# Kernel optimization log

Hardware: AMD Instinct MI355X
Metric: run time of the kernel (lower is better)

## Reference

```python
import jax, jax.numpy as jnp
import numpy as np

DIM = 2048
H = 16           # n_heads
KV = 4           # n_kv_heads
G = H // KV      # gqa factor
CQ = 128         # q_compressed_dim
QN, QR = 96, 32  # q nope / rope head dims
CKV = 128        # kv_compressed_dim
KN, KR = 64, 64  # k nope / rope head dims
VD = 256         # v_head_dim
THETA = 10000.0


def _t5_layer_norm(x, gamma, eps=1e-5):
    mu = jnp.mean(x, axis=-1, keepdims=True)
    var = jnp.var(x, axis=-1, keepdims=True)
    return (x - mu) * jax.lax.rsqrt(var + eps) * gamma


def _rope(x):
    # x: [B, H, S, D] with interleaved even/odd rotation, positions = arange(S)
    S, D = x.shape[-2], x.shape[-1]
    inv_freq = 1.0 / THETA ** (jnp.arange(0, D, 2, dtype=jnp.float32) / D)
    ang = jnp.arange(S, dtype=jnp.float32)[:, None] * inv_freq  # [S, D/2]
    cos = jnp.cos(ang).astype(x.dtype)
    sin = jnp.sin(ang).astype(x.dtype)
    xe, xo = x[..., ::2], x[..., 1::2]
    re = xe * cos - xo * sin
    ro = xe * sin + xo * cos
    return jnp.stack((re, ro), axis=-1).reshape(x.shape)


def setup_inputs() -> dict:
    key = jax.random.key(0)
    ks = jax.random.split(key, 7)
    s = 0.02
    return {
        "x": jax.random.normal(ks[0], (2, 2048, DIM), dtype=jnp.float32),
        "w_dq": jax.random.normal(ks[1], (DIM, CQ), dtype=jnp.float32) * s,
        "gamma_q": jnp.ones((CQ,), dtype=jnp.float32),
        "w_uq": jax.random.normal(ks[2], (CQ, H * (QN + QR)), dtype=jnp.float32) * s,
        "w_dkv": jax.random.normal(ks[3], (DIM, CKV + KR), dtype=jnp.float32) * s,
        "gamma_kv": jnp.ones((CKV,), dtype=jnp.float32),
        "w_ukv": jax.random.normal(ks[4], (CKV, KV * (KN + VD)), dtype=jnp.float32) * s,
        "w_o": jax.random.normal(ks[5], (H * VD, DIM), dtype=jnp.float32) * s,
    }


def reference(x, w_dq, gamma_q, w_uq, w_dkv, gamma_kv, w_ukv, w_o):
    B, S, _ = x.shape
    # low-rank Q path
    cq = _t5_layer_norm(x @ w_dq, gamma_q)                     # [B,S,CQ]
    q = cq @ w_uq                                              # [B,S,H*(QN+QR)]
    q_nope = q[..., : H * QN].reshape(B, S, H, QN).transpose(0, 2, 1, 3)
    q_rope = q[..., H * QN :].reshape(B, S, H, QR).transpose(0, 2, 1, 3)
    q_rope = _rope(q_rope)
    q_states = jnp.concatenate((q_nope, q_rope), axis=-1)      # [B,H,S,QN+QR]

    # low-rank KV path + decoupled shared rope key
    ckv_kr = x @ w_dkv                                         # [B,S,CKV+KR]
    ckv = _t5_layer_norm(ckv_kr[..., :CKV], gamma_kv)
    k_rope = _rope(ckv_kr[..., CKV:][:, None, :, :])           # [B,1,S,KR]
    kv = ckv @ w_ukv                                           # [B,S,KV*(KN+VD)]
    k_nope = kv[..., : KV * KN].reshape(B, S, KV, KN).transpose(0, 2, 1, 3)
    v_states = kv[..., KV * KN :].reshape(B, S, KV, VD).transpose(0, 2, 1, 3)
    k_states = jnp.concatenate(
        (k_nope, jnp.broadcast_to(k_rope, (B, KV, S, KR))), axis=-1
    )                                                          # [B,KV,S,KN+KR]

    # grouped-query attention: broadcast kv heads instead of materializing repeats
    dqk = QN + QR  # == KN + KR == 128
    qg = q_states.reshape(B, KV, G, S, dqk)
    scores = jnp.einsum("bgrqd,bgkd->bgrqk", qg, k_states) / jnp.sqrt(
        jnp.asarray(dqk, dtype=x.dtype)
    )
    causal = jnp.triu(jnp.ones((S, S), dtype=bool), k=1)
    scores = jnp.where(causal, -jnp.inf, scores)
    attn = jax.nn.softmax(scores, axis=-1)
    out = jnp.einsum("bgrqk,bgkv->bgrqv", attn, v_states)      # [B,KV,G,S,VD]
    out = out.reshape(B, H, S, VD).transpose(0, 2, 1, 3).reshape(B, S, H * VD)
    return out @ w_o
```

## Files before the change

### kernel.cpp

```cpp
#include <hip/hip_runtime.h>
#include <hip/hip_bf16.h>
#include <math.h>

#define DIM   2048
#define S_LEN 2048
#define BATCH 2
#define NH    16
#define NKV   4
#define CQ_   128
#define QN_   96
#define QR_   32
#define CKV_  128
#define KN_   64
#define KR_   64
#define VD_   256
#define ROWS_TOT (BATCH*S_LEN)
#define QK_SCALE 0.08838834764831845f
#define LOG2E    1.4426950408889634f

typedef __attribute__((ext_vector_type(8)))  short short8;
typedef __attribute__((ext_vector_type(4)))  short short4v;
typedef __attribute__((ext_vector_type(4)))  float float4v;
typedef __attribute__((ext_vector_type(16))) float float16v;
typedef __attribute__((ext_vector_type(4)))  int   int4v;

__device__ inline short f2bf(float x) {
    union { __hip_bfloat16 h; short s; } u;
    u.h = __float2bfloat16(x);
    return u.s;
}

__device__ __forceinline__ void gl_lds16(const short* g, short* lds) {
    __builtin_amdgcn_global_load_lds(
        (const __attribute__((address_space(1))) unsigned int*)(g),
        (__attribute__((address_space(3))) unsigned int*)(lds),
        16, 0, 0);
}


__global__ __launch_bounds__(256)
void kprep_all(const float* __restrict__ x, const float* __restrict__ w_o,
               const float* __restrict__ w_uq, const float* __restrict__ w_ukv,
               const float* __restrict__ w_dq, const float* __restrict__ w_dkv,
               short* __restrict__ xbf, short* __restrict__ w_oT,
               short* __restrict__ w_uqT, short* __restrict__ w_ukvT,
               short* __restrict__ wdT, float* __restrict__ tq,
               float* __restrict__ tk)
{
    const int bid = blockIdx.x, tid = threadIdx.x;
    if (bid < 4096) {
        int i = bid * 2048 + tid * 8;
        float4 a = *reinterpret_cast<const float4*>(x + i);
        float4 b = *reinterpret_cast<const float4*>(x + i + 4);
        short8 o;
        o[0] = f2bf(a.x); o[1] = f2bf(a.y); o[2] = f2bf(a.z); o[3] = f2bf(a.w);
        o[4] = f2bf(b.x); o[5] = f2bf(b.y); o[6] = f2bf(b.z); o[7] = f2bf(b.w);
        *reinterpret_cast<short8*>(xbf + i) = o;
        return;
    }
    if (bid >= 6408) {
        int gid = (bid - 6408) * 256 + tid;
        int spos = gid / 48, e = gid - spos * 48;
        if (e < 16) {
            float inv = powf(10000.f, -(float)(2 * e) / 32.f);
            float sn, c; sincosf((float)spos * inv, &sn, &c);
            tq[(spos * 16 + e) * 2 + 0] = c;
            tq[(spos * 16 + e) * 2 + 1] = sn;
        } else {
            int i2 = e - 16;
            float inv = powf(10000.f, -(float)(2 * i2) / 64.f);
            float sn, c; sincosf((float)spos * inv, &sn, &c);
            tk[(spos * 32 + i2) * 2 + 0] = c;
            tk[(spos * 32 + i2) * 2 + 1] = sn;
        }
        return;
    }

    __shared__ float tf[64][65];
    const int tb = bid - 4096;
    int lb, nct, R; short* dst;
    if (tb < 2048)      { lb = tb;        nct = 32; R = 4096; dst = w_oT;   }
    else if (tb < 2112) { lb = tb - 2048; nct = 32; R = 128;  dst = w_uqT;  }
    else if (tb < 2152) { lb = tb - 2112; nct = 20; R = 128;  dst = w_ukvT; }
    else                { lb = tb - 2152; nct = 5;  R = 2048; dst = wdT;    }
    const int ct = lb % nct, rt = lb / nct;
    const int r0 = rt * 64, c0 = ct * 64;
    const float* src; int stride, nbase;
    if (tb < 2048)      { src = w_o;   stride = 2048; nbase = c0; }
    else if (tb < 2112) { src = w_uq;  stride = 2048; nbase = c0; }
    else if (tb < 2152) { src = w_ukv; stride = 1280; nbase = c0; }
    else if (ct < 2)    { src = w_dq;  stride = 128;  nbase = c0; }
    else                { src = w_dkv; stride = 192;  nbase = c0 - 128; }

    #pragma unroll
    for (int u4 = 0; u4 < 4; ++u4) {
        int u = u4 * 256 + tid;
        int kr = u >> 4, nc = (u & 15) * 4;
        float4 v = *reinterpret_cast<const float4*>(&src[(size_t)(r0 + kr) * stride + nbase + nc]);
        tf[kr][nc + 0] = v.x; tf[kr][nc + 1] = v.y;
        tf[kr][nc + 2] = v.z; tf[kr][nc + 3] = v.w;
    }
    __syncthreads();
    #pragma unroll
    for (int u2 = 0; u2 < 2; ++u2) {
        int u = u2 * 256 + tid;
        int nr = u >> 3, kc8 = (u & 7) * 8;
        short8 o;
        #pragma unroll
        for (int j = 0; j < 8; ++j) o[j] = f2bf(tf[kc8 + j][nr]);
        *reinterpret_cast<short8*>(&dst[(size_t)(c0 + nr) * R + r0 + kc8]) = o;
    }
}

__global__ __launch_bounds__(256)
void k1_mfma(const short* __restrict__ xbf, const short* __restrict__ wdT,
             const float* __restrict__ gamma_q, const float* __restrict__ gamma_kv,
             const float* __restrict__ tk,
             short* __restrict__ cq_bf, short* __restrict__ ckv_bf,
             float* __restrict__ kr_rope)
{
    __shared__ float ys[16][321];
    __shared__ float st[16][4];
    const int tid = threadIdx.x, lane = tid & 63, w = tid >> 6;
    const int g = lane >> 4, l15 = lane & 15;
    const int m0 = blockIdx.x * 16;
    const int wn0 = w * 80;

    float4v acc[5];
    #pragma unroll
    for (int nj = 0; nj < 5; ++nj) acc[nj] = (float4v){0.f, 0.f, 0.f, 0.f};

    const short* arow = xbf + (size_t)(m0 + l15) * 2048 + g * 8;
    for (int ks = 0; ks < 64; ++ks) {
        short8 a = *reinterpret_cast<const short8*>(arow + ks * 32);
        #pragma unroll
        for (int nj = 0; nj < 5; ++nj) {
            short8 bf = *reinterpret_cast<const short8*>(
                wdT + (size_t)(wn0 + nj * 16 + l15) * 2048 + ks * 32 + g * 8);
            acc[nj] = __builtin_amdgcn_mfma_f32_16x16x32_bf16(a, bf, acc[nj], 0, 0, 0);
        }
    }

    #pragma unroll
    for (int nj = 0; nj < 5; ++nj)
        #pragma unroll
        for (int r = 0; r < 4; ++r)
            ys[g * 4 + r][wn0 + nj * 16 + l15] = acc[nj][r];
    __syncthreads();

    if (tid < 32) {
        int row = tid >> 1, seg = tid & 1, base = seg * 128;
        float s1 = 0.f, s2 = 0.f;
        for (int j = 0; j < 128; ++j) { float v = ys[row][base + j]; s1 += v; s2 += v * v; }
        float mu  = s1 * (1.f / 128.f);
        float var = s2 * (1.f / 128.f) - mu * mu;
        st[row][seg * 2 + 0] = mu;
        st[row][seg * 2 + 1] = rsqrtf(var + 1e-5f);
    }
    __syncthreads();

    for (int i = tid; i < 16 * 320; i += 256) {
        int row = i / 320, col = i - row * 320;
        int r = m0 + row, spos = r & (S_LEN - 1);
        float v = ys[row][col];
        if (col < 128) {
            cq_bf[(size_t)r * CQ_ + col] =
                f2bf((v - st[row][0]) * st[row][1] * gamma_q[col] * (QK_SCALE * LOG2E));
        } else if (col < 256) {
            ckv_bf[(size_t)r * CKV_ + (col - 128)] =
                f2bf((v - st[row][2]) * st[row][3] * gamma_kv[col - 128]);
        } else {
            int d = col - 256, i2 = d >> 1;
            float xe = ys[row][256 + (d & ~1)];
            float xo = ys[row][256 + (d | 1)];
            float c  = tk[(spos * 32 + i2) * 2 + 0];
            float sn = tk[(spos * 32 + i2) * 2 + 1];
            kr_rope[(size_t)r * KR_ + d] = (d & 1) ? (xe * sn + xo * c)
                                                   : (xe * c - xo * sn);
        }
    }
}

__global__ __launch_bounds__(256)
void k23_fused(const short* __restrict__ cq_bf, const short* __restrict__ w_uqT,
               const float* __restrict__ tq, short* __restrict__ q_states,
               const short* __restrict__ ckv_bf, const short* __restrict__ w_ukvT,
               const float* __restrict__ kr_rope,
               short* __restrict__ k_frag, short* __restrict__ v_frag)
{
    const int tid = threadIdx.x, lane = tid & 63, w = tid >> 6;
    const int g = lane >> 4, l15 = lane & 15;

    if (blockIdx.x < 512) {
        const int bm = blockIdx.x >> 1, ns = blockIdx.x & 1;
        const int m0 = bm * 16;
        const int nb = ns * 1024 + w * 256;

        short8 af[4];
        #pragma unroll
        for (int ks = 0; ks < 4; ++ks)
            af[ks] = *reinterpret_cast<const short8*>(
                cq_bf + (size_t)(m0 + l15) * 128 + ks * 32 + g * 8);

        float4v acc[16];
        #pragma unroll
        for (int nj = 0; nj < 16; ++nj) acc[nj] = (float4v){0.f, 0.f, 0.f, 0.f};

        #pragma unroll
        for (int ks = 0; ks < 4; ++ks)
            #pragma unroll
            for (int nj = 0; nj < 16; ++nj) {
                short8 bf = *reinterpret_cast<const short8*>(
                    w_uqT + (size_t)(nb + nj * 16 + l15) * 128 + ks * 32 + g * 8);
                acc[nj] = __builtin_amdgcn_mfma_f32_16x16x32_bf16(af[ks], bf, acc[nj], 0, 0, 0);
            }

        #pragma unroll
        for (int nj = 0; nj < 16; ++nj) {
            int j = nb + nj * 16 + l15;
            if (j < NH * QN_) {
                int h = j / QN_, d = j - h * QN_;
                #pragma unroll
                for (int r = 0; r < 4; ++r) {
                    int rg = m0 + g * 4 + r, bb = rg >> 11, spos = rg & (S_LEN - 1);
                    q_states[(((size_t)bb * NH + h) * S_LEN + spos) * 128 + d] =
                        f2bf(acc[nj][r]);
                }
            } else {
                int jj = j - NH * QN_;
                int h = jj >> 5, d = jj & 31, i2 = d >> 1;
                #pragma unroll
                for (int r = 0; r < 4; ++r) {
                    int rg = m0 + g * 4 + r, bb = rg >> 11, spos = rg & (S_LEN - 1);
                    float v = acc[nj][r];
                    float p = __shfl_xor(v, 1, 64);
                    float c  = tq[(spos * 16 + i2) * 2 + 0];
                    float sn = tq[(spos * 16 + i2) * 2 + 1];
                    float out = (d & 1) ? (p * sn + v * c) : (v * c - p * sn);
                    q_states[(((size_t)bb * NH + h) * S_LEN + spos) * 128 + QN_ + d] =
                        f2bf(out);
                }
            }
        }
    } else {
        const int m0 = (blockIdx.x - 512) * 16;
        const int nb = w * 320;

        short8 af[4];
        #pragma unroll
        for (int ks = 0; ks < 4; ++ks)
            af[ks] = *reinterpret_cast<const short8*>(
                ckv_bf + (size_t)(m0 + l15) * 128 + ks * 32 + g * 8);

        float4v acc[20];
        #pragma unroll
        for (int nj = 0; nj < 20; ++nj) acc[nj] = (float4v){0.f, 0.f, 0.f, 0.f};

        #pragma unroll
        for (int ks = 0; ks < 4; ++ks)
            #pragma unroll
            for (int nj = 0; nj < 20; ++nj) {
                short8 bf = *reinterpret_cast<const short8*>(
                    w_ukvT + (size_t)(nb + nj * 16 + l15) * 128 + ks * 32 + g * 8);
                acc[nj] = __builtin_amdgcn_mfma_f32_16x16x32_bf16(af[ks], bf, acc[nj], 0, 0, 0);
            }

        #pragma unroll
        for (int nj = 0; nj < 20; ++nj) {
            int j = nb + nj * 16 + l15;
            if (j < NKV * KN_) {
                int kvh = j >> 6, d = j & 63;
                int stf = d >> 4, hif = (d >> 3) & 1, jo = d & 7;
                #pragma unroll
                for (int r = 0; r < 4; ++r) {
                    int rg = m0 + g * 4 + r, bb = rg >> 11, spos = rg & (S_LEN - 1);
                    int bk = bb * NKV + kvh;
                    size_t idx = ((size_t)(bk * 32 + (spos >> 6)) * 1024
                                  + ((spos >> 5) & 1) * 512 + stf * 64 + hif * 32
                                  + (spos & 31)) * 8 + jo;
                    k_frag[idx] = f2bf(acc[nj][r]);
                }
            } else {
                int jj = j - NKV * KN_;
                int kvh = jj >> 8, d = jj & 255;
                int dt5 = d >> 5, l31d = d & 31;
                #pragma unroll
                for (int r = 0; r < 4; ++r) {
                    int rg = m0 + g * 4 + r, bb = rg >> 11, spos = rg & (S_LEN - 1);
                    int bk = bb * NKV + kvh;
                    size_t slot = (size_t)(bk * 32 + (spos >> 6)) * 2048
                                  + dt5 * 256 + ((spos & 63) >> 5) * 128
                                  + ((spos >> 4) & 1) * 64 + ((spos >> 3) & 1) * 32 + l31d;
                    v_frag[slot * 8 + (spos & 7)] = f2bf(acc[nj][r]);
                }
            }
        }

        for (int i = tid; i < 16 * KR_; i += 256) {
            int rr = i >> 6, dd = i & 63;
            int rg = m0 + rr, bb = rg >> 11, spos = rg & (S_LEN - 1);
            short vv = f2bf(kr_rope[(size_t)rg * KR_ + dd]);
            int d = 64 + dd;
            int stf = d >> 4, hif = (d >> 3) & 1, jo = d & 7;
            size_t ubase = ((size_t)(spos >> 6)) * 1024
                           + ((spos >> 5) & 1) * 512 + stf * 64 + hif * 32 + (spos & 31);
            #pragma unroll
            for (int kvh = 0; kvh < NKV; ++kvh) {
                int bk = bb * NKV + kvh;
                k_frag[((size_t)bk * 32 * 1024 + ubase) * 8 + jo] = vv;
            }
        }
    }
}

__global__ __launch_bounds__(512, 1)
void k4_attn_mfma(const short* __restrict__ q_states,
                  const short* __restrict__ k_frag,
                  const short* __restrict__ v_frag,
                  short* __restrict__ attn_out)
{
    __shared__ __align__(16) short ks_lds[3][8192];
    __shared__ __align__(16) short vt_lds[2][16384];

    const int tid = threadIdx.x, lane = tid & 63, w = tid >> 6;
    const int l31 = lane & 31, hi = lane >> 5;
    const int g = w & 3, h = w >> 2;
    const int bid = blockIdx.x;
    const int qt = (bid < 256) ? (15 - (bid >> 5)) : (7 - ((bid - 256) >> 5));
    const int bh = bid & 31;
    const int h_head = bh & 15, b = bh >> 4, kvh = h_head >> 2;
    const int bk = b * NKV + kvh;

    const short* kfbase = k_frag + (size_t)bk * 32 * 8192;
    const short* vfbase = v_frag + (size_t)bk * 32 * 16384;

    const int qrow0 = qt * 128 + g * 32;
    const int qglob = qrow0 + l31;

    short8 qcur[8];
    {
        const short* qr = q_states +
            (((size_t)b * NH + h_head) * S_LEN + qrow0 + l31) * 128 + hi * 8;
        #pragma unroll
        for (int st = 0; st < 8; ++st)
            qcur[st] = *reinterpret_cast<const short8*>(qr + st * 16);
    }

    float16v o[8];
    #pragma unroll
    for (int dt = 0; dt < 8; ++dt)
        #pragma unroll
        for (int r = 0; r < 16; ++r) o[dt][r] = 0.f;
    float mreg = -1e30f, lreg = 0.f;

    const int nkt = 2 * (qt + 1);

    auto issueK = [&](int kt, int bufi) {
        const short* src = kfbase + (size_t)kt * 8192;
        #pragma unroll
        for (int i = 0; i < 2; ++i) {
            int c = w * 2 + i;
            gl_lds16(src + c * 512 + lane * 8, &ks_lds[bufi][c * 512]);
        }
    };
    auto issueV = [&](int kt, int bufi) {
        const short* src = vfbase + (size_t)kt * 16384;
        #pragma unroll
        for (int i = 0; i < 4; ++i) {
            int c = w * 4 + i;
            gl_lds16(src + c * 512 + lane * 8, &vt_lds[bufi][c * 512]);
        }
    };

    issueK(0, 0);
    issueV(0, 0);
    issueK(1, 1);

    for (int seq = 0; seq < nkt; ++seq) {
        if (seq < nkt - 1) { asm volatile("s_waitcnt vmcnt(2)" ::: "memory"); }
        else               { asm volatile("s_waitcnt vmcnt(0)" ::: "memory"); }
        __builtin_amdgcn_s_barrier();
        __builtin_amdgcn_sched_barrier(0);

        if (seq + 1 < nkt) issueV(seq + 1, (seq + 1) & 1);
        if (seq + 2 < nkt) issueK(seq + 2, (seq + 2) % 3);

        const int kvb = seq * 64 + h * 32;
        if (kvb <= qrow0 + 31) {
            const short* kbuf = &ks_lds[seq % 3][h * 4096];
            float16v sa, sb;
            #pragma unroll
            for (int r = 0; r < 16; ++r) { sa[r] = 0.f; sb[r] = 0.f; }
            __builtin_amdgcn_s_setprio(1);
            #pragma unroll
            for (int st = 0; st < 8; st += 2) {
                short8 kf0 = *reinterpret_cast<const short8*>(kbuf + st * 512 + lane * 8);
                sa = __builtin_amdgcn_mfma_f32_32x32x16_bf16(kf0, qcur[st], sa, 0, 0, 0);
                short8 kf1 = *reinterpret_cast<const short8*>(kbuf + (st + 1) * 512 + lane * 8);
                sb = __builtin_amdgcn_mfma_f32_32x32x16_bf16(kf1, qcur[st + 1], sb, 0, 0, 0);
            }
            __builtin_amdgcn_s_setprio(0);
            float16v s;
            #pragma unroll
            for (int r = 0; r < 16; ++r) s[r] = sa[r] + sb[r];

            if (kvb + 31 > qglob || kvb + 31 > qrow0 + 31) {
                if (kvb + 31 > qrow0) {
                    #pragma unroll
                    for (int r = 0; r < 16; ++r) {
                        int kc = kvb + ((r & 3) + 8 * (r >> 2) + 4 * hi);
                        if (kc > qglob) s[r] = -1e30f;
                    }
                }
            }

            float mx = s[0];
            #pragma unroll
            for (int r = 1; r < 16; ++r) mx = fmaxf(mx, s[r]);
            mx = fmaxf(mx, __shfl_xor(mx, 32, 64));
            bool need = mx > mreg + 8.f;
            if (__ballot(need)) {
                float mnew = fmaxf(mreg, mx);
                float corr = exp2f(mreg - mnew);
                mreg = mnew;
                lreg *= corr;
                #pragma unroll
                for (int dt = 0; dt < 8; ++dt)
                    #pragma unroll
                    for (int r = 0; r < 16; ++r) o[dt][r] *= corr;
            }
            #pragma unroll
            for (int r = 0; r < 16; ++r) s[r] = exp2f(s[r] - mreg);
            float ps = 0.f;
            #pragma unroll
            for (int r = 0; r < 16; ++r) ps += s[r];
            ps += __shfl_xor(ps, 32, 64);
            lreg += ps;

            const short* vbuf = &vt_lds[seq & 1][h * 1024];
            __builtin_amdgcn_s_setprio(1);
            #pragma unroll
            for (int ks = 0; ks < 2; ++ks) {
                const int rb = ks * 8;
                int c01, c23, c45, c67;
                asm("v_cvt_pk_bf16_f32 %0, %1, %2" : "=v"(c01) : "v"(s[rb+0]), "v"(s[rb+1]));
                asm("v_cvt_pk_bf16_f32 %0, %1, %2" : "=v"(c23) : "v"(s[rb+2]), "v"(s[rb+3]));
                asm("v_cvt_pk_bf16_f32 %0, %1, %2" : "=v"(c45) : "v"(s[rb+4]), "v"(s[rb+5]));
                asm("v_cvt_pk_bf16_f32 %0, %1, %2" : "=v"(c67) : "v"(s[rb+6]), "v"(s[rb+7]));
                asm("v_permlane32_swap_b32 %0, %1" : "+v"(c01), "+v"(c45));
                asm("v_permlane32_swap_b32 %0, %1" : "+v"(c23), "+v"(c67));
                union { int4v i4; short8 s8; } u_;
                u_.i4.x = c01; u_.i4.y = c23; u_.i4.z = c45; u_.i4.w = c67;
                short8 pa = u_.s8;
                #pragma unroll
                for (int dt = 0; dt < 8; ++dt) {
                    short8 vf = *reinterpret_cast<const short8*>(
                        vbuf + dt * 2048 + ks * 512 + lane * 8);
                    o[dt] = __builtin_amdgcn_mfma_f32_32x32x16_bf16(vf, pa, o[dt], 0, 0, 0);
                }
            }
            __builtin_amdgcn_s_setprio(0);
        }
    }

    __syncthreads();
    {
        float* mlb = (float*)(&ks_lds[0][0]);
        mlb[w * 64 + lane] = mreg;
        mlb[512 + w * 64 + lane] = lreg;
    }
    __syncthreads();
    float s0f = 0.f, s1f = 0.f;
    if (h == 0) {
        float* mlb = (float*)(&ks_lds[0][0]);
        float m1 = mlb[(w + 4) * 64 + lane];
        float l1 = mlb[512 + (w + 4) * 64 + lane];
        float ms = fmaxf(mreg, m1);
        float c0 = exp2f(mreg - ms), c1 = exp2f(m1 - ms);
        float ls = lreg * c0 + l1 * c1;
        s0f = c0 / ls; s1f = c1 / ls;
    }
    float* cb = (float*)(&ks_lds[0][0]) + 1024;
    short* obase = attn_out + (((size_t)b * S_LEN + qglob) * NH + h_head) * VD_;
    for (int dt = 0; dt < 8; ++dt) {
        __syncthreads();
        if (h == 1) {
            #pragma unroll
            for (int r = 0; r < 16; ++r)
                cb[r * 256 + g * 64 + lane] = o[dt][r];
        }
        __syncthreads();
        if (h == 0) {
            #pragma unroll
            for (int r = 0; r < 16; ++r)
                o[dt][r] = o[dt][r] * s0f + cb[r * 256 + g * 64 + lane] * s1f;
            #pragma unroll
            for (int k4i = 0; k4i < 4; ++k4i) {
                int d0 = dt * 32 + k4i * 8 + hi * 4;
                short4v pk;
                #pragma unroll
                for (int j = 0; j < 4; ++j) pk[j] = f2bf(o[dt][k4i * 4 + j]);
                *reinterpret_cast<short4v*>(obase + d0) = pk;
            }
        }
    }
}

__global__ __launch_bounds__(256)
void k5_gemm_mfma(const short* __restrict__ A,
                  const short* __restrict__ Bt,
                  float* __restrict__ C)
{
    __shared__ __align__(16) short at[128 * 64];
    __shared__ __align__(16) short bt[128 * 64];
    const int tid  = threadIdx.x;
    const int lane = tid & 63;
    const int wid  = tid >> 6;
    const int wm = wid >> 1, wn = wid & 1;
    const int g = lane >> 4, l15 = lane & 15;
    const int swz = (blockIdx.x & 7) * 64 + (blockIdx.x >> 3);
    const int bm = swz & 31, bn = swz >> 5;
    const int m0 = bm * 128, n0 = bn * 128;

    float4v acc[4][4];
    #pragma unroll
    for (int mi = 0; mi < 4; ++mi)
        #pragma unroll
        for (int nj = 0; nj < 4; ++nj) acc[mi][nj] = (float4v){0.f, 0.f, 0.f, 0.f};

    for (int k0 = 0; k0 < 4096; k0 += 64) {
        __syncthreads();
        #pragma unroll
        for (int i = 0; i < 4; ++i) {
            int row = wid * 32 + i * 8 + (lane >> 3);
            int ch  = lane & 7;
            gl_lds16(A + (size_t)(m0 + row) * 4096 + k0 + ((ch ^ (row & 7)) * 8),
                     at + wid * 2048 + i * 512);
            gl_lds16(Bt + (size_t)(n0 + row) * 4096 + k0 + ((ch ^ (row & 7)) * 8),
                     bt + wid * 2048 + i * 512);
        }
        __syncthreads();

        #pragma unroll
        for (int kb = 0; kb < 2; ++kb) {
            short8 af[4], bfr[4];
            #pragma unroll
            for (int mi = 0; mi < 4; ++mi) {
                int row = wm * 64 + mi * 16 + l15;
                af[mi] = *reinterpret_cast<const short8*>(
                    at + row * 64 + (((g + 4 * kb) ^ (row & 7)) * 8));
            }
            #pragma unroll
            for (int nj = 0; nj < 4; ++nj) {
                int row = wn * 64 + nj * 16 + l15;
                bfr[nj] = *reinterpret_cast<const short8*>(
                    bt + row * 64 + (((g + 4 * kb) ^ (row & 7)) * 8));
            }
            #pragma unroll
            for (int mi = 0; mi < 4; ++mi)
                #pragma unroll
                for (int nj = 0; nj < 4; ++nj)
                    acc[mi][nj] = __builtin_amdgcn_mfma_f32_16x16x32_bf16(
                        af[mi], bfr[nj], acc[mi][nj], 0, 0, 0);
        }
    }

    #pragma unroll
    for (int mi = 0; mi < 4; ++mi)
        #pragma unroll
        for (int nj = 0; nj < 4; ++nj)
            #pragma unroll
            for (int r = 0; r < 4; ++r)
                C[(size_t)(m0 + wm * 64 + mi * 16 + g * 4 + r) * DIM + n0 + wn * 64 + nj * 16 + l15] =
                    acc[mi][nj][r];
}

extern "C" void kernel_launch(void* const* d_in, const int* in_sizes, int n_in,
                              void* d_out, int out_size, void* d_ws, size_t ws_size,
                              hipStream_t stream)
{
    const float* x        = (const float*)d_in[0];
    const float* w_dq     = (const float*)d_in[1];
    const float* gamma_q  = (const float*)d_in[2];
    const float* w_uq     = (const float*)d_in[3];
    const float* w_dkv    = (const float*)d_in[4];
    const float* gamma_kv = (const float*)d_in[5];
    const float* w_ukv    = (const float*)d_in[6];
    const float* w_o      = (const float*)d_in[7];
    float* out = (float*)d_out;

    char* ws = (char*)d_ws;
    float* kr_rope  = (float*)(ws);
    short* cq_bf    = (short*)(ws + (1ull  << 20));
    short* ckv_bf   = (short*)(ws + (2ull  << 20));
    float* tq       = (float*)(ws + (3ull  << 20));
    float* tk       = (float*)(ws + (4ull  << 20));
    short* w_uqT    = (short*)(ws + (5ull  << 20));
    short* w_ukvT   = (short*)(ws + (6ull  << 20));
    short* wdT      = (short*)(ws + (7ull  << 20));
    short* q_states = (short*)(ws + (9ull  << 20));
    short* k_frag   = (short*)(ws + (25ull << 20));
    short* v_frag   = (short*)(ws + (29ull << 20));
    short* attn_out = (short*)(ws + (37ull << 20));
    short* w_oT     = (short*)(ws + (69ull << 20));
    short* xbf      = (short*)(ws + (85ull << 20));

    kprep_all<<<dim3(6792), dim3(256), 0, stream>>>(
        x, w_o, w_uq, w_ukv, w_dq, w_dkv,
        xbf, w_oT, w_uqT, w_ukvT, wdT, tq, tk);

    k1_mfma<<<dim3(ROWS_TOT / 16), dim3(256), 0, stream>>>(
        xbf, wdT, gamma_q, gamma_kv, tk, cq_bf, ckv_bf, kr_rope);

    k23_fused<<<dim3(768), dim3(256), 0, stream>>>(
        cq_bf, w_uqT, tq, q_states, ckv_bf, w_ukvT, kr_rope, k_frag, v_frag);

    k4_attn_mfma<<<dim3(512), dim3(512), 0, stream>>>(
        q_states, k_frag, v_frag, attn_out);

    k5_gemm_mfma<<<dim3(512), dim3(256), 0, stream>>>(
        attn_out, w_oT, out);
}
```

Before: 269.0 us.

## Absorb KV up-projection into Q and output weights for latent-space attention

Measured after the change: 236.1 us (median of 2 runs). 1.14x faster.

```diff
diff --git a/kernel.cpp b/kernel.cpp
--- a/kernel.cpp
+++ b/kernel.cpp
@@ -14,6 +14,8 @@
 #define KN_   64
 #define KR_   64
 #define VD_   256
+#define DQK   192
+#define DV    128
 #define ROWS_TOT (BATCH*S_LEN)
 #define QK_SCALE 0.08838834764831845f
 #define LOG2E    1.4426950408889634f
@@ -37,29 +39,26 @@
         16, 0, 0);
 }
 
+__device__ __forceinline__ short8 cast8(const float* p) {
+    float4 a = *reinterpret_cast<const float4*>(p);
+    float4 b = *reinterpret_cast<const float4*>(p + 4);
+    short8 o;
+    o[0] = f2bf(a.x); o[1] = f2bf(a.y); o[2] = f2bf(a.z); o[3] = f2bf(a.w);
+    o[4] = f2bf(b.x); o[5] = f2bf(b.y); o[6] = f2bf(b.z); o[7] = f2bf(b.w);
+    return o;
+}
+
 
 __global__ __launch_bounds__(256)
-void kprep_all(const float* __restrict__ x, const float* __restrict__ w_o,
-               const float* __restrict__ w_uq, const float* __restrict__ w_ukv,
+void kprep_all(const float* __restrict__ w_o, const float* __restrict__ w_uq,
                const float* __restrict__ w_dq, const float* __restrict__ w_dkv,
-               short* __restrict__ xbf, short* __restrict__ w_oT,
-               short* __restrict__ w_uqT, short* __restrict__ w_ukvT,
+               short* __restrict__ w_oT, short* __restrict__ w_uqT,
                short* __restrict__ wdT, float* __restrict__ tq,
                float* __restrict__ tk)
 {
     const int bid = blockIdx.x, tid = threadIdx.x;
-    if (bid < 4096) {
-        int i = bid * 2048 + tid * 8;
-        float4 a = *reinterpret_cast<const float4*>(x + i);
-        float4 b = *reinterpret_cast<const float4*>(x + i + 4);
-        short8 o;
-        o[0] = f2bf(a.x); o[1] = f2bf(a.y); o[2] = f2bf(a.z); o[3] = f2bf(a.w);
-        o[4] = f2bf(b.x); o[5] = f2bf(b.y); o[6] = f2bf(b.z); o[7] = f2bf(b.w);
-        *reinterpret_cast<short8*>(xbf + i) = o;
-        return;
-    }
-    if (bid >= 6408) {
-        int gid = (bid - 6408) * 256 + tid;
+    if (bid >= 2272) {
+        int gid = (bid - 2272) * 256 + tid;
         int spos = gid / 48, e = gid - spos * 48;
         if (e < 16) {
             float inv = powf(10000.f, -(float)(2 * e) / 32.f);
@@ -77,20 +76,18 @@
     }
 
     __shared__ float tf[64][65];
-    const int tb = bid - 4096;
     int lb, nct, R; short* dst;
-    if (tb < 2048)      { lb = tb;        nct = 32; R = 4096; dst = w_oT;   }
-    else if (tb < 2112) { lb = tb - 2048; nct = 32; R = 128;  dst = w_uqT;  }
-    else if (tb < 2152) { lb = tb - 2112; nct = 20; R = 128;  dst = w_ukvT; }
-    else                { lb = tb - 2152; nct = 5;  R = 2048; dst = wdT;    }
+    if (bid < 160)      { lb = bid;       nct = 5;  R = 2048; dst = wdT;   }
+    else if (bid < 224) { lb = bid - 160; nct = 32; R = 128;  dst = w_uqT; }
+    else                { lb = bid - 224; nct = 32; R = 4096; dst = w_oT;  }
     const int ct = lb % nct, rt = lb / nct;
     const int r0 = rt * 64, c0 = ct * 64;
     const float* src; int stride, nbase;
-    if (tb < 2048)      { src = w_o;   stride = 2048; nbase = c0; }
-    else if (tb < 2112) { src = w_uq;  stride = 2048; nbase = c0; }
-    else if (tb < 2152) { src = w_ukv; stride = 1280; nbase = c0; }
-    else if (ct < 2)    { src = w_dq;  stride = 128;  nbase = c0; }
-    else                { src = w_dkv; stride = 192;  nbase = c0 - 128; }
+    if (bid < 160) {
+        if (ct < 2) { src = w_dq;  stride = 128; nbase = c0; }
+        else        { src = w_dkv; stride = 192; nbase = c0 - 128; }
+    } else if (bid < 224) { src = w_uq; stride = 2048; nbase = c0; }
+    else                  { src = w_o;  stride = 2048; nbase = c0; }
 
     #pragma unroll
     for (int u4 = 0; u4 < 4; ++u4) {
@@ -113,11 +110,94 @@
 }
 
 __global__ __launch_bounds__(256)
-void k1_mfma(const short* __restrict__ xbf, const short* __restrict__ wdT,
+void kcomb(const float* __restrict__ w_uq, const float* __restrict__ w_ukv,
+           const short* __restrict__ w_oT,
+           short* __restrict__ WqcombT, short* __restrict__ WcombT)
+{
+    const int tid = threadIdx.x, lane = tid & 63, wid = tid >> 6;
+    const int g = lane >> 4, l15 = lane & 15;
+
+    if (blockIdx.x < 16) {
+        const int h = blockIdx.x, kvh = h >> 2;
+        float4v acc[2][8];
+        #pragma unroll
+        for (int mi = 0; mi < 2; ++mi)
+            #pragma unroll
+            for (int nj = 0; nj < 8; ++nj) acc[mi][nj] = (float4v){0.f, 0.f, 0.f, 0.f};
+        #pragma unroll
+        for (int kb = 0; kb < 2; ++kb) {
+            short8 af[2], bf[8];
+            #pragma unroll
+            for (int mi = 0; mi < 2; ++mi) {
+                int j = wid * 32 + mi * 16 + l15;
+                af[mi] = cast8(&w_ukv[(size_t)j * 1280 + kvh * 64 + kb * 32 + g * 8]);
+            }
+            #pragma unroll
+            for (int nj = 0; nj < 8; ++nj) {
+                int e = nj * 16 + l15;
+                bf[nj] = cast8(&w_uq[(size_t)e * 2048 + h * 96 + kb * 32 + g * 8]);
+            }
+            #pragma unroll
+            for (int mi = 0; mi < 2; ++mi)
+                #pragma unroll
+                for (int nj = 0; nj < 8; ++nj)
+                    acc[mi][nj] = __builtin_amdgcn_mfma_f32_16x16x32_bf16(
+                        af[mi], bf[nj], acc[mi][nj], 0, 0, 0);
+        }
+        #pragma unroll
+        for (int mi = 0; mi < 2; ++mi)
+            #pragma unroll
+            for (int nj = 0; nj < 8; ++nj)
+                #pragma unroll
+                for (int r = 0; r < 4; ++r)
+                    WqcombT[(size_t)h * 16384 + (wid * 32 + mi * 16 + g * 4 + r) * 128
+                            + nj * 16 + l15] = f2bf(acc[mi][nj][r]);
+    } else {
+        const int bb = blockIdx.x - 16;
+        const int h = bb >> 4, nt = bb & 15, kvh = h >> 2;
+        const int wm = wid >> 1, wn = wid & 1;
+        float4v acc[4][4];
+        #pragma unroll
+        for (int mi = 0; mi < 4; ++mi)
+            #pragma unroll
+            for (int nj = 0; nj < 4; ++nj) acc[mi][nj] = (float4v){0.f, 0.f, 0.f, 0.f};
+        for (int kb = 0; kb < 8; ++kb) {
+            short8 af[4], bf[4];
+            #pragma unroll
+            for (int mi = 0; mi < 4; ++mi) {
+                int n = nt * 128 + wm * 64 + mi * 16 + l15;
+                af[mi] = *reinterpret_cast<const short8*>(
+                    &w_oT[(size_t)n * 4096 + h * 256 + kb * 32 + g * 8]);
+            }
+            #pragma unroll
+            for (int nj = 0; nj < 4; ++nj) {
+                int c = wn * 64 + nj * 16 + l15;
+                bf[nj] = cast8(&w_ukv[(size_t)c * 1280 + 256 + kvh * 256 + kb * 32 + g * 8]);
+            }
+            #pragma unroll
+            for (int mi = 0; mi < 4; ++mi)
+                #pragma unroll
+                for (int nj = 0; nj < 4; ++nj)
+                    acc[mi][nj] = __builtin_amdgcn_mfma_f32_16x16x32_bf16(
+                        af[mi], bf[nj], acc[mi][nj], 0, 0, 0);
+        }
+        #pragma unroll
+        for (int mi = 0; mi < 4; ++mi)
+            #pragma unroll
+            for (int nj = 0; nj < 4; ++nj)
+                #pragma unroll
+                for (int r = 0; r < 4; ++r)
+                    WcombT[(size_t)(nt * 128 + wm * 64 + mi * 16 + g * 4 + r) * 2048
+                           + h * 128 + wn * 64 + nj * 16 + l15] = f2bf(acc[mi][nj][r]);
+    }
+}
+
+__global__ __launch_bounds__(256)
+void k1_mfma(const float* __restrict__ x, const short* __restrict__ wdT,
              const float* __restrict__ gamma_q, const float* __restrict__ gamma_kv,
              const float* __restrict__ tk,
-             short* __restrict__ cq_bf, short* __restrict__ ckv_bf,
-             float* __restrict__ kr_rope)
+             short* __restrict__ cq_bf, short* __restrict__ kimg,
+             short* __restrict__ vimg)
 {
     __shared__ float ys[16][321];
     __shared__ float st[16][4];
@@ -130,9 +210,9 @@
     #pragma unroll
     for (int nj = 0; nj < 5; ++nj) acc[nj] = (float4v){0.f, 0.f, 0.f, 0.f};
 
-    const short* arow = xbf + (size_t)(m0 + l15) * 2048 + g * 8;
+    const float* arow = x + (size_t)(m0 + l15) * 2048 + g * 8;
     for (int ks = 0; ks < 64; ++ks) {
-        short8 a = *reinterpret_cast<const short8*>(arow + ks * 32);
+        short8 a = cast8(arow + ks * 32);
         #pragma unroll
         for (int nj = 0; nj < 5; ++nj) {
             short8 bf = *reinterpret_cast<const short8*>(
@@ -159,155 +239,97 @@
     }
     __syncthreads();
 
-    for (int i = tid; i < 16 * 320; i += 256) {
-        int row = i / 320, col = i - row * 320;
-        int r = m0 + row, spos = r & (S_LEN - 1);
-        float v = ys[row][col];
-        if (col < 128) {
-            cq_bf[(size_t)r * CQ_ + col] =
-                f2bf((v - st[row][0]) * st[row][1] * gamma_q[col] * (QK_SCALE * LOG2E));
-        } else if (col < 256) {
-            ckv_bf[(size_t)r * CKV_ + (col - 128)] =
-                f2bf((v - st[row][2]) * st[row][3] * gamma_kv[col - 128]);
+    for (int i = tid; i < 16 * 128; i += 256) {
+        int row = i >> 7, col = i & 127;
+        int r = m0 + row;
+        cq_bf[(size_t)r * CQ_ + col] =
+            f2bf((ys[row][col] - st[row][0]) * st[row][1] * gamma_q[col] * (QK_SCALE * LOG2E));
+    }
+    for (int i = tid; i < 16 * 192; i += 256) {
+        int row = i / 192, d = i - row * 192;
+        int r = m0 + row, b = r >> 11, spos = r & (S_LEN - 1);
+        int tile = b * 32 + (spos >> 6);
+        float val;
+        if (d < 128) {
+            val = (ys[row][128 + d] - st[row][2]) * st[row][3] * gamma_kv[d];
+            short v_ = f2bf(val);
+            size_t vslot = (d >> 5) * 256 + ((spos >> 5) & 1) * 128
+                           + ((spos >> 4) & 1) * 64 + ((spos >> 3) & 1) * 32 + (d & 31);
+            vimg[((size_t)tile * 1024 + vslot) * 8 + (spos & 7)] = v_;
+            size_t kslot = ((spos >> 5) & 1) * 768 + (d >> 4) * 64
+                           + ((d >> 3) & 1) * 32 + (spos & 31);
+            kimg[((size_t)tile * 1536 + kslot) * 8 + (d & 7)] = v_;
         } else {
-            int d = col - 256, i2 = d >> 1;
-            float xe = ys[row][256 + (d & ~1)];
-            float xo = ys[row][256 + (d | 1)];
+            int dd = d - 128, i2 = dd >> 1;
+            float xe = ys[row][256 + (dd & ~1)];
+            float xo = ys[row][256 + (dd | 1)];
             float c  = tk[(spos * 32 + i2) * 2 + 0];
             float sn = tk[(spos * 32 + i2) * 2 + 1];
-            kr_rope[(size_t)r * KR_ + d] = (d & 1) ? (xe * sn + xo * c)
-                                                   : (xe * c - xo * sn);
+            val = (dd & 1) ? (xe * sn + xo * c) : (xe * c - xo * sn);
+            size_t kslot = ((spos >> 5) & 1) * 768 + (d >> 4) * 64
+                           + ((d >> 3) & 1) * 32 + (spos & 31);
+            kimg[((size_t)tile * 1536 + kslot) * 8 + (d & 7)] = f2bf(val);
         }
     }
 }
 
 __global__ __launch_bounds__(256)
-void k23_fused(const short* __restrict__ cq_bf, const short* __restrict__ w_uqT,
-               const float* __restrict__ tq, short* __restrict__ q_states,
-               const short* __restrict__ ckv_bf, const short* __restrict__ w_ukvT,
-               const float* __restrict__ kr_rope,
-               short* __restrict__ k_frag, short* __restrict__ v_frag)
+void k2_mfma(const short* __restrict__ cq_bf, const short* __restrict__ WqcombT,
+             const short* __restrict__ w_uqT, const float* __restrict__ tq,
+             short* __restrict__ q_states)
 {
     const int tid = threadIdx.x, lane = tid & 63, w = tid >> 6;
     const int g = lane >> 4, l15 = lane & 15;
-
-    if (blockIdx.x < 512) {
-        const int bm = blockIdx.x >> 1, ns = blockIdx.x & 1;
-        const int m0 = bm * 16;
-        const int nb = ns * 1024 + w * 256;
-
-        short8 af[4];
-        #pragma unroll
-        for (int ks = 0; ks < 4; ++ks)
-            af[ks] = *reinterpret_cast<const short8*>(
-                cq_bf + (size_t)(m0 + l15) * 128 + ks * 32 + g * 8);
-
-        float4v acc[16];
-        #pragma unroll
-        for (int nj = 0; nj < 16; ++nj) acc[nj] = (float4v){0.f, 0.f, 0.f, 0.f};
-
-        #pragma unroll
-        for (int ks = 0; ks < 4; ++ks)
-            #pragma unroll
-            for (int nj = 0; nj < 16; ++nj) {
-                short8 bf = *reinterpret_cast<const short8*>(
-                    w_uqT + (size_t)(nb + nj * 16 + l15) * 128 + ks * 32 + g * 8);
-                acc[nj] = __builtin_amdgcn_mfma_f32_16x16x32_bf16(af[ks], bf, acc[nj], 0, 0, 0);
-            }
-
+    const int bm = blockIdx.x / 3, ns = blockIdx.x % 3;
+    const int m0 = bm * 16;
+    const int nb = ns * 1024 + w * 256;
+
+    short8 af[4];
+    #pragma unroll
+    for (int ks = 0; ks < 4; ++ks)
+        af[ks] = *reinterpret_cast<const short8*>(
+            cq_bf + (size_t)(m0 + l15) * 128 + ks * 32 + g * 8);
+
+    float4v acc[16];
+    #pragma unroll
+    for (int nj = 0; nj < 16; ++nj) acc[nj] = (float4v){0.f, 0.f, 0.f, 0.f};
+
+    #pragma unroll
+    for (int ks = 0; ks < 4; ++ks)
         #pragma unroll
         for (int nj = 0; nj < 16; ++nj) {
             int j = nb + nj * 16 + l15;
-            if (j < NH * QN_) {
-                int h = j / QN_, d = j - h * QN_;
-                #pragma unroll
-                for (int r = 0; r < 4; ++r) {
-                    int rg = m0 + g * 4 + r, bb = rg >> 11, spos = rg & (S_LEN - 1);
-                    q_states[(((size_t)bb * NH + h) * S_LEN + spos) * 128 + d] =
-                        f2bf(acc[nj][r]);
-                }
-            } else {
-                int jj = j - NH * QN_;
-                int h = jj >> 5, d = jj & 31, i2 = d >> 1;
-                #pragma unroll
-                for (int r = 0; r < 4; ++r) {
-                    int rg = m0 + g * 4 + r, bb = rg >> 11, spos = rg & (S_LEN - 1);
-                    float v = acc[nj][r];
-                    float p = __shfl_xor(v, 1, 64);
-                    float c  = tq[(spos * 16 + i2) * 2 + 0];
-                    float sn = tq[(spos * 16 + i2) * 2 + 1];
-                    float out = (d & 1) ? (p * sn + v * c) : (v * c - p * sn);
-                    q_states[(((size_t)bb * NH + h) * S_LEN + spos) * 128 + QN_ + d] =
-                        f2bf(out);
-                }
-            }
-        }
-    } else {
-        const int m0 = (blockIdx.x - 512) * 16;
-        const int nb = w * 320;
-
-        short8 af[4];
-        #pragma unroll
-        for (int ks = 0; ks < 4; ++ks)
-            af[ks] = *reinterpret_cast<const short8*>(
-                ckv_bf + (size_t)(m0 + l15) * 128 + ks * 32 + g * 8);
-
-        float4v acc[20];
-        #pragma unroll
-        for (int nj = 0; nj < 20; ++nj) acc[nj] = (float4v){0.f, 0.f, 0.f, 0.f};
-
-        #pragma unroll
-        for (int ks = 0; ks < 4; ++ks)
-            #pragma unroll
-            for (int nj = 0; nj < 20; ++nj) {
-                short8 bf = *reinterpret_cast<const short8*>(
-                    w_ukvT + (size_t)(nb + nj * 16 + l15) * 128 + ks * 32 + g * 8);
-                acc[nj] = __builtin_amdgcn_mfma_f32_16x16x32_bf16(af[ks], bf, acc[nj], 0, 0, 0);
-            }
-
-        #pragma unroll
-        for (int nj = 0; nj < 20; ++nj) {
-            int j = nb + nj * 16 + l15;
-            if (j < NKV * KN_) {
-                int kvh = j >> 6, d = j & 63;
-                int stf = d >> 4, hif = (d >> 3) & 1, jo = d & 7;
-                #pragma unroll
-                for (int r = 0; r < 4; ++r) {
-                    int rg = m0 + g * 4 + r, bb = rg >> 11, spos = rg & (S_LEN - 1);
-                    int bk = bb * NKV + kvh;
-                    size_t idx = ((size_t)(bk * 32 + (spos >> 6)) * 1024
-                                  + ((spos >> 5) & 1) * 512 + stf * 64 + hif * 32
-                                  + (spos & 31)) * 8 + jo;
-                    k_frag[idx] = f2bf(acc[nj][r]);
-                }
-            } else {
-                int jj = j - NKV * KN_;
-                int kvh = jj >> 8, d = jj & 255;
-                int dt5 = d >> 5, l31d = d & 31;
-                #pragma unroll
-                for (int r = 0; r < 4; ++r) {
-                    int rg = m0 + g * 4 + r, bb = rg >> 11, spos = rg & (S_LEN - 1);
-                    int bk = bb * NKV + kvh;
-                    size_t slot = (size_t)(bk * 32 + (spos >> 6)) * 2048
-                                  + dt5 * 256 + ((spos & 63) >> 5) * 128
-                                  + ((spos >> 4) & 1) * 64 + ((spos >> 3) & 1) * 32 + l31d;
-                    v_frag[slot * 8 + (spos & 7)] = f2bf(acc[nj][r]);
-                }
-            }
-        }
-
-        for (int i = tid; i < 16 * KR_; i += 256) {
-            int rr = i >> 6, dd = i & 63;
-            int rg = m0 + rr, bb = rg >> 11, spos = rg & (S_LEN - 1);
-            short vv = f2bf(kr_rope[(size_t)rg * KR_ + dd]);
-            int d = 64 + dd;
-            int stf = d >> 4, hif = (d >> 3) & 1, jo = d & 7;
-            size_t ubase = ((size_t)(spos >> 6)) * 1024
-                           + ((spos >> 5) & 1) * 512 + stf * 64 + hif * 32 + (spos & 31);
-            #pragma unroll
-            for (int kvh = 0; kvh < NKV; ++kvh) {
-                int bk = bb * NKV + kvh;
-                k_frag[((size_t)bk * 32 * 1024 + ubase) * 8 + jo] = vv;
+            int h = j / 192, t = j - h * 192;
+            const short* brow;
+            if (t < 128)       brow = WqcombT + (size_t)h * 16384 + (size_t)t * 128;
+            else if (t < 160)  brow = w_uqT + (size_t)(h * 96 + 64 + (t - 128)) * 128;
+            else               brow = w_uqT + (size_t)(1536 + h * 32 + (t - 160)) * 128;
+            short8 bf = *reinterpret_cast<const short8*>(brow + ks * 32 + g * 8);
+            acc[nj] = __builtin_amdgcn_mfma_f32_16x16x32_bf16(af[ks], bf, acc[nj], 0, 0, 0);
+        }
+
+    #pragma unroll
+    for (int nj = 0; nj < 16; ++nj) {
+        int j = nb + nj * 16 + l15;
+        int h = j / 192, t = j - h * 192;
+        if (t < 160) {
+            #pragma unroll
+            for (int r = 0; r < 4; ++r) {
+                int rg = m0 + g * 4 + r, bb = rg >> 11, spos = rg & (S_LEN - 1);
+                q_states[((size_t)(bb * NH + h) * S_LEN + spos) * DQK + t] =
+                    f2bf(acc[nj][r]);
+            }
+        } else {
+            int dd = t - 160, i2 = dd >> 1;
+            #pragma unroll
+            for (int r = 0; r < 4; ++r) {
+                int rg = m0 + g * 4 + r, bb = rg >> 11, spos = rg & (S_LEN - 1);
+                float v = acc[nj][r];
+                float p = __shfl_xor(v, 1, 64);
+                float c  = tq[(spos * 16 + i2) * 2 + 0];
+                float sn = tq[(spos * 16 + i2) * 2 + 1];
+                float out = (dd & 1) ? (p * sn + v * c) : (v * c - p * sn);
+                q_states[((size_t)(bb * NH + h) * S_LEN + spos) * DQK + t] = f2bf(out);
             }
         }
     }
@@ -315,40 +337,39 @@
 
 __global__ __launch_bounds__(512, 1)
 void k4_attn_mfma(const short* __restrict__ q_states,
-                  const short* __restrict__ k_frag,
-                  const short* __restrict__ v_frag,
+                  const short* __restrict__ kimg,
+                  const short* __restrict__ vimg,
                   short* __restrict__ attn_out)
 {
-    __shared__ __align__(16) short ks_lds[3][8192];
-    __shared__ __align__(16) short vt_lds[2][16384];
+    __shared__ __align__(16) short ks_lds[3][12288];
+    __shared__ __align__(16) short vt_lds[2][8192];
 
     const int tid = threadIdx.x, lane = tid & 63, w = tid >> 6;
+    const int bid = blockIdx.x;
     const int l31 = lane & 31, hi = lane >> 5;
     const int g = w & 3, h = w >> 2;
-    const int bid = blockIdx.x;
     const int qt = (bid < 256) ? (15 - (bid >> 5)) : (7 - ((bid - 256) >> 5));
     const int bh = bid & 31;
-    const int h_head = bh & 15, b = bh >> 4, kvh = h_head >> 2;
-    const int bk = b * NKV + kvh;
-
-    const short* kfbase = k_frag + (size_t)bk * 32 * 8192;
-    const short* vfbase = v_frag + (size_t)bk * 32 * 16384;
+    const int h_head = bh & 15, b = bh >> 4;
+
+    const short* kfbase = kimg + (size_t)b * 32 * 12288;
+    const short* vfbase = vimg + (size_t)b * 32 * 8192;
 
     const int qrow0 = qt * 128 + g * 32;
     const int qglob = qrow0 + l31;
 
-    short8 qcur[8];
+    short8 qcur[12];
     {
         const short* qr = q_states +
-            (((size_t)b * NH + h_head) * S_LEN + qrow0 + l31) * 128 + hi * 8;
-        #pragma unroll
-        for (int st = 0; st < 8; ++st)
+            ((size_t)(b * NH + h_head) * S_LEN + qglob) * DQK + hi * 8;
+        #pragma unroll
+        for (int st = 0; st < 12; ++st)
             qcur[st] = *reinterpret_cast<const short8*>(qr + st * 16);
     }
 
-    float16v o[8];
-    #pragma unroll
-    for (int dt = 0; dt < 8; ++dt)
+    float16v o[4];
+    #pragma unroll
+    for (int dt = 0; dt < 4; ++dt)
         #pragma unroll
         for (int r = 0; r < 16; ++r) o[dt][r] = 0.f;
     float mreg = -1e30f, lreg = 0.f;
@@ -356,18 +377,18 @@
     const int nkt = 2 * (qt + 1);
 
     auto issueK = [&](int kt, int bufi) {
-        const short* src = kfbase + (size_t)kt * 8192;
+        const short* src = kfbase + (size_t)kt * 12288;
+        #pragma unroll
+        for (int i = 0; i < 3; ++i) {
+            int c = w * 3 + i;
+            gl_lds16(src + c * 512 + lane * 8, &ks_lds[bufi][c * 512]);
+        }
+    };
+    auto issueV = [&](int kt, int bufi) {
+        const short* src = vfbase + (size_t)kt * 8192;
         #pragma unroll
         for (int i = 0; i < 2; ++i) {
             int c = w * 2 + i;
-            gl_lds16(src + c * 512 + lane * 8, &ks_lds[bufi][c * 512]);
-        }
-    };
-    auto issueV = [&](int kt, int bufi) {
-        const short* src = vfbase + (size_t)kt * 16384;
-        #pragma unroll
-        for (int i = 0; i < 4; ++i) {
-            int c = w * 4 + i;
             gl_lds16(src + c * 512 + lane * 8, &vt_lds[bufi][c * 512]);
         }
     };
@@ -377,7 +398,7 @@
     issueK(1, 1);
 
     for (int seq = 0; seq < nkt; ++seq) {
-        if (seq < nkt - 1) { asm volatile("s_waitcnt vmcnt(2)" ::: "memory"); }
+        if (seq < nkt - 1) { asm volatile("s_waitcnt vmcnt(3)" ::: "memory"); }
         else               { asm volatile("s_waitcnt vmcnt(0)" ::: "memory"); }
         __builtin_amdgcn_s_barrier();
         __builtin_amdgcn_sched_barrier(0);
@@ -387,13 +408,13 @@
 
         const int kvb = seq * 64 + h * 32;
         if (kvb <= qrow0 + 31) {
-            const short* kbuf = &ks_lds[seq % 3][h * 4096];
+            const short* kbuf = &ks_lds[seq % 3][h * 6144];
             float16v sa, sb;
             #pragma unroll
             for (int r = 0; r < 16; ++r) { sa[r] = 0.f; sb[r] = 0.f; }
             __builtin_amdgcn_s_setprio(1);
             #pragma unroll
-            for (int st = 0; st < 8; st += 2) {
+            for (int st = 0; st < 12; st += 2) {
                 short8 kf0 = *reinterpret_cast<const short8*>(kbuf + st * 512 + lane * 8);
                 sa = __builtin_amdgcn_mfma_f32_32x32x16_bf16(kf0, qcur[st], sa, 0, 0, 0);
                 short8 kf1 = *reinterpret_cast<const short8*>(kbuf + (st + 1) * 512 + lane * 8);
@@ -404,13 +425,11 @@
             #pragma unroll
             for (int r = 0; r < 16; ++r) s[r] = sa[r] + sb[r];
 
-            if (kvb + 31 > qglob || kvb + 31 > qrow0 + 31) {
-                if (kvb + 31 > qrow0) {
-                    #pragma unroll
-                    for (int r = 0; r < 16; ++r) {
-                        int kc = kvb + ((r & 3) + 8 * (r >> 2) + 4 * hi);
-                        if (kc > qglob) s[r] = -1e30f;
-                    }
+            if (kvb + 31 > qrow0) {
+                #pragma unroll
+                for (int r = 0; r < 16; ++r) {
+                    int kc = kvb + ((r & 3) + 8 * (r >> 2) + 4 * hi);
+                    if (kc > qglob) s[r] = -1e30f;
                 }
             }
 
@@ -425,7 +444,7 @@
                 mreg = mnew;
                 lreg *= corr;
                 #pragma unroll
-                for (int dt = 0; dt < 8; ++dt)
+                for (int dt = 0; dt < 4; ++dt)
                     #pragma unroll
                     for (int r = 0; r < 16; ++r) o[dt][r] *= corr;
             }
@@ -453,7 +472,7 @@
                 u_.i4.x = c01; u_.i4.y = c23; u_.i4.z = c45; u_.i4.w = c67;
                 short8 pa = u_.s8;
                 #pragma unroll
-                for (int dt = 0; dt < 8; ++dt) {
+                for (int dt = 0; dt < 4; ++dt) {
                     short8 vf = *reinterpret_cast<const short8*>(
                         vbuf + dt * 2048 + ks * 512 + lane * 8);
                     o[dt] = __builtin_amdgcn_mfma_f32_32x32x16_bf16(vf, pa, o[dt], 0, 0, 0);
@@ -481,8 +500,8 @@
         s0f = c0 / ls; s1f = c1 / ls;
     }
     float* cb = (float*)(&ks_lds[0][0]) + 1024;
-    short* obase = attn_out + (((size_t)b * S_LEN + qglob) * NH + h_head) * VD_;
-    for (int dt = 0; dt < 8; ++dt) {
+    short* obase = attn_out + ((size_t)(b * S_LEN + qglob)) * 2048 + h_head * 128;
+    for (int dt = 0; dt < 4; ++dt) {
         __syncthreads();
         if (h == 1) {
             #pragma unroll
@@ -518,8 +537,8 @@
     const int wid  = tid >> 6;
     const int wm = wid >> 1, wn = wid & 1;
     const int g = lane >> 4, l15 = lane & 15;
-    const int swz = (blockIdx.x & 7) * 64 + (blockIdx.x >> 3);
-    const int bm = swz & 31, bn = swz >> 5;
+    const int wg = (blockIdx.x & 7) * 64 + (blockIdx.x >> 3);
+    const int bn = wg & 15, bm = wg >> 4;
     const int m0 = bm * 128, n0 = bn * 128;
 
     float4v acc[4][4];
@@ -528,15 +547,15 @@
         #pragma unroll
         for (int nj = 0; nj < 4; ++nj) acc[mi][nj] = (float4v){0.f, 0.f, 0.f, 0.f};
 
-    for (int k0 = 0; k0 < 4096; k0 += 64) {
+    for (int k0 = 0; k0 < 2048; k0 += 64) {
         __syncthreads();
         #pragma unroll
         for (int i = 0; i < 4; ++i) {
             int row = wid * 32 + i * 8 + (lane >> 3);
             int ch  = lane & 7;
-            gl_lds16(A + (size_t)(m0 + row) * 4096 + k0 + ((ch ^ (row & 7)) * 8),
+            gl_lds16(A + (size_t)(m0 + row) * 2048 + k0 + ((ch ^ (row & 7)) * 8),
                      at + wid * 2048 + i * 512);
-            gl_lds16(Bt + (size_t)(n0 + row) * 4096 + k0 + ((ch ^ (row & 7)) * 8),
+            gl_lds16(Bt + (size_t)(n0 + row) * 2048 + k0 + ((ch ^ (row & 7)) * 8),
                      bt + wid * 2048 + i * 512);
         }
         __syncthreads();
@@ -590,34 +609,34 @@
     float* out = (float*)d_out;
 
     char* ws = (char*)d_ws;
-    float* kr_rope  = (float*)(ws);
-    short* cq_bf    = (short*)(ws + (1ull  << 20));
-    short* ckv_bf   = (short*)(ws + (2ull  << 20));
-    float* tq       = (float*)(ws + (3ull  << 20));
-    float* tk       = (float*)(ws + (4ull  << 20));
-    short* w_uqT    = (short*)(ws + (5ull  << 20));
-    short* w_ukvT   = (short*)(ws + (6ull  << 20));
-    short* wdT      = (short*)(ws + (7ull  << 20));
-    short* q_states = (short*)(ws + (9ull  << 20));
-    short* k_frag   = (short*)(ws + (25ull << 20));
-    short* v_frag   = (short*)(ws + (29ull << 20));
-    short* attn_out = (short*)(ws + (37ull << 20));
-    short* w_oT     = (short*)(ws + (69ull << 20));
-    short* xbf      = (short*)(ws + (85ull << 20));
-
-    kprep_all<<<dim3(6792), dim3(256), 0, stream>>>(
-        x, w_o, w_uq, w_ukv, w_dq, w_dkv,
-        xbf, w_oT, w_uqT, w_ukvT, wdT, tq, tk);
+    short* cq_bf    = (short*)(ws);
+    float* tq       = (float*)(ws + (1ull  << 20));
+    float* tk       = (float*)(ws + (2ull  << 20));
+    short* w_uqT    = (short*)(ws + (3ull  << 20));
+    short* wdT      = (short*)(ws + (4ull  << 20));
+    short* WqcombT  = (short*)(ws + (6ull  << 20));
+    short* kimg     = (short*)(ws + (7ull  << 20));
+    short* vimg     = (short*)(ws + (9ull  << 20));
+    short* q_states = (short*)(ws + (11ull << 20));
+    short* attn_out = (short*)(ws + (38ull << 20));
+    short* w_oT     = (short*)(ws + (54ull << 20));
+    short* WcombT   = (short*)(ws + (70ull << 20));
+
+    kprep_all<<<dim3(2656), dim3(256), 0, stream>>>(
+        w_o, w_uq, w_dq, w_dkv, w_oT, w_uqT, wdT, tq, tk);
+
+    kcomb<<<dim3(272), dim3(256), 0, stream>>>(
+        w_uq, w_ukv, w_oT, WqcombT, WcombT);
 
     k1_mfma<<<dim3(ROWS_TOT / 16), dim3(256), 0, stream>>>(
-        xbf, wdT, gamma_q, gamma_kv, tk, cq_bf, ckv_bf, kr_rope);
-
-    k23_fused<<<dim3(768), dim3(256), 0, stream>>>(
-        cq_bf, w_uqT, tq, q_states, ckv_bf, w_ukvT, kr_rope, k_frag, v_frag);
+        x, wdT, gamma_q, gamma_kv, tk, cq_bf, kimg, vimg);
+
+    k2_mfma<<<dim3((ROWS_TOT / 16) * 3), dim3(256), 0, stream>>>(
+        cq_bf, WqcombT, w_uqT, tq, q_states);
 
     k4_attn_mfma<<<dim3(512), dim3(512), 0, stream>>>(
-        q_states, k_frag, v_frag, attn_out);
+        q_states, kimg, vimg, attn_out);
 
     k5_gemm_mfma<<<dim3(512), dim3(256), 0, stream>>>(
-        attn_out, w_oT, out);
-}
+        attn_out, WcombT, out);
+}
```
